# Kernel tuning notes

Hardware: AMD Instinct MI355X
Metric: run time of the kernel (lower is better)

Reference implementation:

```python
import jax, jax.numpy as jnp
import numpy as np
from jax import lax

B = 32768
IMG = 28
K = 3
OUT_HW = IMG - K + 1  # 26
FLAT = OUT_HW * OUT_HW  # 676
HID = 300
NCLS = 10


def setup_inputs() -> dict:
    key = jax.random.key(0)
    ks = jax.random.split(key, 8)
    x = jax.random.normal(ks[0], (B, IMG * IMG), dtype=jnp.float32)
    conv_w = jax.random.normal(ks[1], (K, K), dtype=jnp.float32) * 0.1
    # Linear params stored as (in, out) so forward is h @ W + b
    W1 = jax.random.normal(ks[2], (FLAT, HID), dtype=jnp.float32) * 0.04
    b1 = jnp.zeros((HID,), dtype=jnp.float32)
    W2 = jax.random.normal(ks[3], (HID, HID), dtype=jnp.float32) * 0.06
    b2 = jnp.zeros((HID,), dtype=jnp.float32)
    W3 = jax.random.normal(ks[4], (HID, NCLS), dtype=jnp.float32) * 0.06
    b3 = jnp.zeros((NCLS,), dtype=jnp.float32)
    return {"x": x, "conv_w": conv_w, "W1": W1, "b1": b1,
            "W2": W2, "b2": b2, "W3": W3, "b3": b3}


def reference(x, conv_w, W1, b1, W2, b2, W3, b3):
    b = x.shape[0]
    img = x.reshape(b, 1, IMG, IMG)  # NCHW
    # Valid cross-correlation with 3x3 kernel -> [B,1,26,26]
    y = lax.conv_general_dilated(
        img, conv_w[None, None, :, :], window_strides=(1, 1), padding="VALID",
        dimension_numbers=("NCHW", "OIHW", "NCHW"))
    h = y.reshape(b, FLAT)
    h = jax.nn.relu(h @ W1 + b1)
    h = jax.nn.relu(h @ W2 + b2)
    return h @ W3 + b3
```

## Files before the change

kernel.cpp:

```cpp
#include <hip/hip_runtime.h>


typedef __bf16 bf16_t;
typedef __bf16 bf16x4 __attribute__((ext_vector_type(4)));
typedef __bf16 bf16x8 __attribute__((ext_vector_type(8)));
typedef float  f32x4  __attribute__((ext_vector_type(4)));

#define MFMA16(a, b, c) __builtin_amdgcn_mfma_f32_16x16x32_bf16((a), (b), (c), 0, 0, 0)

#define W1F_ELEMS (25 * 20 * 64 * 8)
#define W2F_ELEMS (10 * 20 * 64 * 8)
#define W3F_ELEMS (10 * 1 * 64 * 8)
#define ASTRIDE   136

__global__ void prep_weights(const float* __restrict__ conv_w,
                             const float* __restrict__ W1,
                             const float* __restrict__ W2,
                             const float* __restrict__ W3,
                             bf16_t* __restrict__ W1f,
                             bf16_t* __restrict__ W2f,
                             bf16_t* __restrict__ W3f) {
    int idx = blockIdx.x * 256 + threadIdx.x;
    if (idx < 800 * 320) {
        int k = idx / 320;
        int n = idx - k * 320;
        float v = 0.0f;
        if (k < 784 && n < 300) {
            int py = k / 28;
            int px = k - py * 28;
#pragma unroll
            for (int ky = 0; ky < 3; ++ky) {
                int oy = py - ky;
                if (oy < 0 || oy > 25) continue;
#pragma unroll
                for (int kx = 0; kx < 3; ++kx) {
                    int ox = px - kx;
                    if (ox < 0 || ox > 25) continue;
                    v += conv_w[ky * 3 + kx] * W1[(oy * 26 + ox) * 300 + n];
                }
            }
        }
        int kc = k >> 5, quad = (k >> 3) & 3, j = k & 7;
        int nt = n >> 4, nin = n & 15;
        W1f[(((kc * 20 + nt) * 64 + quad * 16 + nin) << 3) + j] = (bf16_t)v;
    } else if (idx < 800 * 320 + 320 * 320) {
        int i2 = idx - 800 * 320;
        int k = i2 / 320;
        int n = i2 - k * 320;
        float v = (k < 300 && n < 300) ? W2[k * 300 + n] : 0.0f;
        int kc = k >> 5, quad = (k >> 3) & 3, j = k & 7;
        int nt = n >> 4, nin = n & 15;
        W2f[(((kc * 20 + nt) * 64 + quad * 16 + nin) << 3) + j] = (bf16_t)v;
    } else if (idx < 800 * 320 + 320 * 320 + 320 * 16) {
        int i3 = idx - (800 * 320 + 320 * 320);
        int k = i3 / 16;
        int n = i3 - k * 16;
        float v = (k < 300 && n < 10) ? W3[k * 10 + n] : 0.0f;
        int kc = k >> 5, quad = (k >> 3) & 3, j = k & 7;
        W3f[(((kc * 64) + quad * 16 + n) << 3) + j] = (bf16_t)v;
    }
}

__device__ __forceinline__ void stage16(const bf16x8* g, bf16x8* l) {
    __builtin_amdgcn_global_load_lds(
        (const __attribute__((address_space(1))) void*)g,
        (__attribute__((address_space(3))) void*)l, 16, 0, 0);
}

__global__ __launch_bounds__(512, 4) void fused_mlp(
    const float* __restrict__ x, const float* __restrict__ b1,
    const float* __restrict__ b2, const float* __restrict__ b3,
    const bf16x8* __restrict__ W1f, const bf16x8* __restrict__ W2f,
    const bf16x8* __restrict__ W3f, float* __restrict__ out) {
    __shared__ bf16x8 bufB1[2 * 1280];
    __shared__ bf16_t Abuf[64 * ASTRIDE];
    __shared__ bf16x8 bufB2[1280];

    bf16x8* hbuf = bufB1;

    const int tid = threadIdx.x;
    const int w   = tid >> 6;
    const int l   = tid & 63;
    const int mh  = w & 1;
    const int nq  = w >> 1;
    const int q   = l >> 4;
    const int l15 = l & 15;
    const int r0  = blockIdx.x * 64;

    const int srow = tid >> 5;
    const int sc4  = tid & 31;
    const int trow = tid >> 3;
    const int tc4  = tid & 7;

    for (int t = w; t < 20; t += 8) stage16(W1f + (t * 64 + l), bufB1 + t * 64);
    for (int t = w; t < 20; t += 8) stage16(W2f + (t * 64 + l), bufB2 + t * 64);

    float4 pf[4];
#pragma unroll
    for (int i = 0; i < 4; ++i)
        pf[i] = *(const float4*)(x + (size_t)(r0 + i * 16 + srow) * 784 + sc4 * 4);

    f32x4 acc[2][5];
#pragma unroll
    for (int m = 0; m < 2; ++m)
#pragma unroll
        for (int nt = 0; nt < 5; ++nt) acc[m][nt] = (f32x4){0.f, 0.f, 0.f, 0.f};

    int kc = 0;
    for (int band = 0; band < 7; ++band) {
        __syncthreads();

        if (band < 6) {
#pragma unroll
            for (int i = 0; i < 4; ++i) {
                bf16x4 v;
                v[0] = (bf16_t)pf[i].x; v[1] = (bf16_t)pf[i].y;
                v[2] = (bf16_t)pf[i].z; v[3] = (bf16_t)pf[i].w;
                *(bf16x4*)&Abuf[(i * 16 + srow) * ASTRIDE + sc4 * 4] = v;
            }
        } else {
            bf16x4 v;
            v[0] = (bf16_t)pf[0].x; v[1] = (bf16_t)pf[0].y;
            v[2] = (bf16_t)pf[0].z; v[3] = (bf16_t)pf[0].w;
            *(bf16x4*)&Abuf[trow * ASTRIDE + tc4 * 4] = v;
        }

        if (band + 1 < 6) {
#pragma unroll
            for (int i = 0; i < 4; ++i)
                pf[i] = *(const float4*)(x + (size_t)(r0 + i * 16 + srow) * 784 +
                                         (band + 1) * 128 + sc4 * 4);
        } else if (band + 1 == 6) {
            pf[0] = (tc4 < 4)
                ? *(const float4*)(x + (size_t)(r0 + trow) * 784 + 768 + tc4 * 4)
                : make_float4(0.f, 0.f, 0.f, 0.f);
        }

        const int nch = (band < 6) ? 4 : 1;
        for (int kcl = 0; kcl < nch; ++kcl, ++kc) {
            __syncthreads();

            if (kc + 1 < 25) {
                int s1 = (kc + 1) & 1;
                for (int t = w; t < 20; t += 8)
                    stage16(W1f + (((kc + 1) * 20 + t) * 64 + l),
                            bufB1 + s1 * 1280 + t * 64);
            }

            bf16x8 afA = *(const bf16x8*)&Abuf[(mh * 32 + l15) * ASTRIDE +
                                               kcl * 32 + q * 8];
            bf16x8 afB = *(const bf16x8*)&Abuf[(mh * 32 + 16 + l15) * ASTRIDE +
                                               kcl * 32 + q * 8];
            const bf16x8* bb = bufB1 + (kc & 1) * 1280 + (nq * 5) * 64 + l;
#pragma unroll
            for (int nt = 0; nt < 5; ++nt) {
                bf16x8 b = bb[nt * 64];
                acc[0][nt] = MFMA16(afA, b, acc[0][nt]);
                acc[1][nt] = MFMA16(afB, b, acc[1][nt]);
            }
        }
    }
    __syncthreads();

    {
        bf16_t* hb = (bf16_t*)hbuf;
#pragma unroll
        for (int nt = 0; nt < 5; ++nt) {
            int n = (nq * 5 + nt) * 16 + l15;
            float bias = (n < 300) ? b1[n] : 0.0f;
            int kc2 = n >> 5, quad = (n >> 3) & 3, j = n & 7;
#pragma unroll
            for (int mt2 = 0; mt2 < 2; ++mt2) {
                int mt = mh * 2 + mt2;
#pragma unroll
                for (int r = 0; r < 4; ++r) {
                    float v = acc[mt2][nt][r] + bias;
                    v = v > 0.f ? v : 0.f;
                    hb[(((kc2 * 4 + mt) * 64 + quad * 16 + q * 4 + r) << 3) + j] =
                        (bf16_t)v;
                }
            }
        }
    }
    __syncthreads();

#pragma unroll
    for (int m = 0; m < 2; ++m)
#pragma unroll
        for (int nt = 0; nt < 5; ++nt) acc[m][nt] = (f32x4){0.f, 0.f, 0.f, 0.f};
    for (int kc2 = 0; kc2 < 10; ++kc2) {
        bf16x8 a0 = hbuf[(kc2 * 4 + mh * 2 + 0) * 64 + l];
        bf16x8 a1 = hbuf[(kc2 * 4 + mh * 2 + 1) * 64 + l];
        const bf16x8* bb = bufB2 + (nq * 5) * 64 + l;
#pragma unroll
        for (int nt = 0; nt < 5; ++nt) {
            bf16x8 b = bb[nt * 64];
            acc[0][nt] = MFMA16(a0, b, acc[0][nt]);
            acc[1][nt] = MFMA16(a1, b, acc[1][nt]);
        }
        if (kc2 + 1 < 10) {
            __syncthreads();
            for (int t = w; t < 20; t += 8)
                stage16(W2f + (((kc2 + 1) * 20 + t) * 64 + l), bufB2 + t * 64);
            __syncthreads();
        }
    }
    __syncthreads();

    {
        bf16_t* hb = (bf16_t*)hbuf;
#pragma unroll
        for (int nt = 0; nt < 5; ++nt) {
            int n = (nq * 5 + nt) * 16 + l15;
            float bias = (n < 300) ? b2[n] : 0.0f;
            int kc2 = n >> 5, quad = (n >> 3) & 3, j = n & 7;
#pragma unroll
            for (int mt2 = 0; mt2 < 2; ++mt2) {
                int mt = mh * 2 + mt2;
#pragma unroll
                for (int r = 0; r < 4; ++r) {
                    float v = acc[mt2][nt][r] + bias;
                    v = v > 0.f ? v : 0.f;
                    hb[(((kc2 * 4 + mt) * 64 + quad * 16 + q * 4 + r) << 3) + j] =
                        (bf16_t)v;
                }
            }
        }
    }
    __syncthreads();

    if (w < 4) {
        f32x4 acc3 = (f32x4){0.f, 0.f, 0.f, 0.f};
#pragma unroll
        for (int kc3 = 0; kc3 < 10; ++kc3)
            acc3 = MFMA16(hbuf[(kc3 * 4 + w) * 64 + l], W3f[kc3 * 64 + l], acc3);
        if (l15 < 10) {
            float bias = b3[l15];
#pragma unroll
            for (int r = 0; r < 4; ++r)
                out[(size_t)(r0 + w * 16 + q * 4 + r) * 10 + l15] = acc3[r] + bias;
        }
    }
}

extern "C" void kernel_launch(void* const* d_in, const int* in_sizes, int n_in,
                              void* d_out, int out_size, void* d_ws, size_t ws_size,
                              hipStream_t stream) {
    const float* x      = (const float*)d_in[0];
    const float* conv_w = (const float*)d_in[1];
    const float* W1     = (const float*)d_in[2];
    const float* b1     = (const float*)d_in[3];
    const float* W2     = (const float*)d_in[4];
    const float* b2     = (const float*)d_in[5];
    const float* W3     = (const float*)d_in[6];
    const float* b3     = (const float*)d_in[7];
    float* out = (float*)d_out;

    char* ws = (char*)d_ws;
    bf16_t* W1f = (bf16_t*)(ws);
    bf16_t* W2f = (bf16_t*)(ws + (size_t)W1F_ELEMS * 2);
    bf16_t* W3f = (bf16_t*)(ws + (size_t)(W1F_ELEMS + W2F_ELEMS) * 2);
    if (ws_size < (size_t)(W1F_ELEMS + W2F_ELEMS + W3F_ELEMS) * 2) return;

    int prep_total = 800 * 320 + 320 * 320 + 320 * 16;
    prep_weights<<<(prep_total + 255) / 256, 256, 0, stream>>>(
        conv_w, W1, W2, W3, W1f, W2f, W3f);

    fused_mlp<<<32768 / 64, 512, 0, stream>>>(
        x, b1, b2, b3, (const bf16x8*)W1f, (const bf16x8*)W2f,
        (const bf16x8*)W3f, out);
}
```

Baseline: 187.5 us.

## Double rows per block and load weights directly into registers instead of LDS

Each block now handles 128 rows instead of 64, with each wave computing a 4x5 tile of MFMA outputs. Weight fragments for W1 and W2 are read straight from global memory (L2-resident) into registers, replacing the LDS staging, double buffering and extra barriers. LDS is merged into a single arena used for both activations and hidden layers. This raises per-wave register use, halves the block count to 256 and lowers occupancy to 2 blocks per CU. The MFMA work is no longer waiting on LDS weight staging, but each wave now issues its own global weight loads with no prefetch overlap.

```diff
diff --git a/kernel.cpp b/kernel.cpp
--- a/kernel.cpp
+++ b/kernel.cpp
@@ -61,58 +61,46 @@
     }
 }
 
-__device__ __forceinline__ void stage16(const bf16x8* g, bf16x8* l) {
-    __builtin_amdgcn_global_load_lds(
-        (const __attribute__((address_space(1))) void*)g,
-        (__attribute__((address_space(3))) void*)l, 16, 0, 0);
-}
-
-__global__ __launch_bounds__(512, 4) void fused_mlp(
+__global__ __launch_bounds__(512, 2) void fused_mlp(
     const float* __restrict__ x, const float* __restrict__ b1,
     const float* __restrict__ b2, const float* __restrict__ b3,
     const bf16x8* __restrict__ W1f, const bf16x8* __restrict__ W2f,
     const bf16x8* __restrict__ W3f, float* __restrict__ out) {
-    __shared__ bf16x8 bufB1[2 * 1280];
-    __shared__ bf16_t Abuf[64 * ASTRIDE];
-    __shared__ bf16x8 bufB2[1280];
-
-    bf16x8* hbuf = bufB1;
+    __shared__ bf16x8 arena[5120];
 
     const int tid = threadIdx.x;
     const int w   = tid >> 6;
     const int l   = tid & 63;
-    const int mh  = w & 1;
-    const int nq  = w >> 1;
     const int q   = l >> 4;
     const int l15 = l & 15;
-    const int r0  = blockIdx.x * 64;
+    const int mq  = w >> 2;
+    const int nq  = w & 3;
+    const int r0  = blockIdx.x * 128;
 
     const int srow = tid >> 5;
     const int sc4  = tid & 31;
-    const int trow = tid >> 3;
-    const int tc4  = tid & 7;
-
-    for (int t = w; t < 20; t += 8) stage16(W1f + (t * 64 + l), bufB1 + t * 64);
-    for (int t = w; t < 20; t += 8) stage16(W2f + (t * 64 + l), bufB2 + t * 64);
-
-    float4 pf[4];
-#pragma unroll
-    for (int i = 0; i < 4; ++i)
+    const int trow = tid >> 2;
+    const int tc4  = tid & 3;
+
+    bf16_t* Abuf = (bf16_t*)arena;
+
+    float4 pf[8];
+#pragma unroll
+    for (int i = 0; i < 8; ++i)
         pf[i] = *(const float4*)(x + (size_t)(r0 + i * 16 + srow) * 784 + sc4 * 4);
 
-    f32x4 acc[2][5];
-#pragma unroll
-    for (int m = 0; m < 2; ++m)
-#pragma unroll
-        for (int nt = 0; nt < 5; ++nt) acc[m][nt] = (f32x4){0.f, 0.f, 0.f, 0.f};
-
-    int kc = 0;
+    f32x4 acc1[4][5];
+#pragma unroll
+    for (int mt = 0; mt < 4; ++mt)
+#pragma unroll
+        for (int nt = 0; nt < 5; ++nt) acc1[mt][nt] = (f32x4){0.f, 0.f, 0.f, 0.f};
+
     for (int band = 0; band < 7; ++band) {
         __syncthreads();
 
         if (band < 6) {
 #pragma unroll
-            for (int i = 0; i < 4; ++i) {
+            for (int i = 0; i < 8; ++i) {
                 bf16x4 v;
                 v[0] = (bf16_t)pf[i].x; v[1] = (bf16_t)pf[i].y;
                 v[2] = (bf16_t)pf[i].z; v[3] = (bf16_t)pf[i].w;
@@ -123,60 +111,54 @@
             v[0] = (bf16_t)pf[0].x; v[1] = (bf16_t)pf[0].y;
             v[2] = (bf16_t)pf[0].z; v[3] = (bf16_t)pf[0].w;
             *(bf16x4*)&Abuf[trow * ASTRIDE + tc4 * 4] = v;
-        }
+            bf16x4 z = (bf16x4){(bf16_t)0.f, (bf16_t)0.f, (bf16_t)0.f, (bf16_t)0.f};
+            *(bf16x4*)&Abuf[trow * ASTRIDE + 16 + tc4 * 4] = z;
+        }
+        __syncthreads();
 
         if (band + 1 < 6) {
 #pragma unroll
-            for (int i = 0; i < 4; ++i)
+            for (int i = 0; i < 8; ++i)
                 pf[i] = *(const float4*)(x + (size_t)(r0 + i * 16 + srow) * 784 +
                                          (band + 1) * 128 + sc4 * 4);
         } else if (band + 1 == 6) {
-            pf[0] = (tc4 < 4)
-                ? *(const float4*)(x + (size_t)(r0 + trow) * 784 + 768 + tc4 * 4)
-                : make_float4(0.f, 0.f, 0.f, 0.f);
+            pf[0] = *(const float4*)(x + (size_t)(r0 + trow) * 784 + 768 + tc4 * 4);
         }
 
         const int nch = (band < 6) ? 4 : 1;
-        for (int kcl = 0; kcl < nch; ++kcl, ++kc) {
-            __syncthreads();
-
-            if (kc + 1 < 25) {
-                int s1 = (kc + 1) & 1;
-                for (int t = w; t < 20; t += 8)
-                    stage16(W1f + (((kc + 1) * 20 + t) * 64 + l),
-                            bufB1 + s1 * 1280 + t * 64);
-            }
-
-            bf16x8 afA = *(const bf16x8*)&Abuf[(mh * 32 + l15) * ASTRIDE +
-                                               kcl * 32 + q * 8];
-            bf16x8 afB = *(const bf16x8*)&Abuf[(mh * 32 + 16 + l15) * ASTRIDE +
-                                               kcl * 32 + q * 8];
-            const bf16x8* bb = bufB1 + (kc & 1) * 1280 + (nq * 5) * 64 + l;
-#pragma unroll
-            for (int nt = 0; nt < 5; ++nt) {
-                bf16x8 b = bb[nt * 64];
-                acc[0][nt] = MFMA16(afA, b, acc[0][nt]);
-                acc[1][nt] = MFMA16(afB, b, acc[1][nt]);
+        for (int kcl = 0; kcl < nch; ++kcl) {
+            const int kc = band * 4 + kcl;
+            bf16x8 bfr[5];
+            const bf16x8* wb = W1f + ((size_t)kc * 20 + nq * 5) * 64 + l;
+#pragma unroll
+            for (int nt = 0; nt < 5; ++nt) bfr[nt] = wb[nt * 64];
+#pragma unroll
+            for (int mt = 0; mt < 4; ++mt) {
+                bf16x8 a = *(const bf16x8*)&Abuf[(mq * 64 + mt * 16 + l15) * ASTRIDE +
+                                                 kcl * 32 + q * 8];
+#pragma unroll
+                for (int nt = 0; nt < 5; ++nt)
+                    acc1[mt][nt] = MFMA16(a, bfr[nt], acc1[mt][nt]);
             }
         }
     }
     __syncthreads();
 
     {
-        bf16_t* hb = (bf16_t*)hbuf;
+        bf16_t* hb = (bf16_t*)arena;
 #pragma unroll
         for (int nt = 0; nt < 5; ++nt) {
-            int n = (nq * 5 + nt) * 16 + l15;
+            int n = nq * 80 + nt * 16 + l15;
             float bias = (n < 300) ? b1[n] : 0.0f;
             int kc2 = n >> 5, quad = (n >> 3) & 3, j = n & 7;
 #pragma unroll
-            for (int mt2 = 0; mt2 < 2; ++mt2) {
-                int mt = mh * 2 + mt2;
+            for (int mt = 0; mt < 4; ++mt) {
+                int mtg = mq * 4 + mt;
 #pragma unroll
                 for (int r = 0; r < 4; ++r) {
-                    float v = acc[mt2][nt][r] + bias;
+                    float v = acc1[mt][nt][r] + bias;
                     v = v > 0.f ? v : 0.f;
-                    hb[(((kc2 * 4 + mt) * 64 + quad * 16 + q * 4 + r) << 3) + j] =
+                    hb[(((kc2 * 8 + mtg) * 64 + quad * 16 + q * 4 + r) << 3) + j] =
                         (bf16_t)v;
                 }
             }
@@ -184,44 +166,41 @@
     }
     __syncthreads();
 
-#pragma unroll
-    for (int m = 0; m < 2; ++m)
-#pragma unroll
-        for (int nt = 0; nt < 5; ++nt) acc[m][nt] = (f32x4){0.f, 0.f, 0.f, 0.f};
-    for (int kc2 = 0; kc2 < 10; ++kc2) {
-        bf16x8 a0 = hbuf[(kc2 * 4 + mh * 2 + 0) * 64 + l];
-        bf16x8 a1 = hbuf[(kc2 * 4 + mh * 2 + 1) * 64 + l];
-        const bf16x8* bb = bufB2 + (nq * 5) * 64 + l;
+    f32x4 acc2[4][5];
+#pragma unroll
+    for (int mt = 0; mt < 4; ++mt)
+#pragma unroll
+        for (int nt = 0; nt < 5; ++nt) acc2[mt][nt] = (f32x4){0.f, 0.f, 0.f, 0.f};
+    for (int kc = 0; kc < 10; ++kc) {
+        bf16x8 b2f[5];
+        const bf16x8* wb = W2f + ((size_t)kc * 20 + nq * 5) * 64 + l;
+#pragma unroll
+        for (int nt = 0; nt < 5; ++nt) b2f[nt] = wb[nt * 64];
+#pragma unroll
+        for (int mt = 0; mt < 4; ++mt) {
+            bf16x8 a = arena[(kc * 8 + mq * 4 + mt) * 64 + l];
+#pragma unroll
+            for (int nt = 0; nt < 5; ++nt)
+                acc2[mt][nt] = MFMA16(a, b2f[nt], acc2[mt][nt]);
+        }
+    }
+    __syncthreads();
+
+    {
+        bf16_t* hb = (bf16_t*)arena;
 #pragma unroll
         for (int nt = 0; nt < 5; ++nt) {
-            bf16x8 b = bb[nt * 64];
-            acc[0][nt] = MFMA16(a0, b, acc[0][nt]);
-            acc[1][nt] = MFMA16(a1, b, acc[1][nt]);
-        }
-        if (kc2 + 1 < 10) {
-            __syncthreads();
-            for (int t = w; t < 20; t += 8)
-                stage16(W2f + (((kc2 + 1) * 20 + t) * 64 + l), bufB2 + t * 64);
-            __syncthreads();
-        }
-    }
-    __syncthreads();
-
-    {
-        bf16_t* hb = (bf16_t*)hbuf;
-#pragma unroll
-        for (int nt = 0; nt < 5; ++nt) {
-            int n = (nq * 5 + nt) * 16 + l15;
+            int n = nq * 80 + nt * 16 + l15;
             float bias = (n < 300) ? b2[n] : 0.0f;
             int kc2 = n >> 5, quad = (n >> 3) & 3, j = n & 7;
 #pragma unroll
-            for (int mt2 = 0; mt2 < 2; ++mt2) {
-                int mt = mh * 2 + mt2;
+            for (int mt = 0; mt < 4; ++mt) {
+                int mtg = mq * 4 + mt;
 #pragma unroll
                 for (int r = 0; r < 4; ++r) {
-                    float v = acc[mt2][nt][r] + bias;
+                    float v = acc2[mt][nt][r] + bias;
                     v = v > 0.f ? v : 0.f;
-                    hb[(((kc2 * 4 + mt) * 64 + quad * 16 + q * 4 + r) << 3) + j] =
+                    hb[(((kc2 * 8 + mtg) * 64 + quad * 16 + q * 4 + r) << 3) + j] =
                         (bf16_t)v;
                 }
             }
@@ -229,17 +208,15 @@
     }
     __syncthreads();
 
-    if (w < 4) {
-        f32x4 acc3 = (f32x4){0.f, 0.f, 0.f, 0.f};
-#pragma unroll
-        for (int kc3 = 0; kc3 < 10; ++kc3)
-            acc3 = MFMA16(hbuf[(kc3 * 4 + w) * 64 + l], W3f[kc3 * 64 + l], acc3);
-        if (l15 < 10) {
-            float bias = b3[l15];
-#pragma unroll
-            for (int r = 0; r < 4; ++r)
-                out[(size_t)(r0 + w * 16 + q * 4 + r) * 10 + l15] = acc3[r] + bias;
-        }
+    f32x4 acc3 = (f32x4){0.f, 0.f, 0.f, 0.f};
+#pragma unroll
+    for (int kc = 0; kc < 10; ++kc)
+        acc3 = MFMA16(arena[(kc * 8 + w) * 64 + l], W3f[kc * 64 + l], acc3);
+    if (l15 < 10) {
+        float bias = b3[l15];
+#pragma unroll
+        for (int r = 0; r < 4; ++r)
+            out[(size_t)(r0 + w * 16 + q * 4 + r) * 10 + l15] = acc3[r] + bias;
     }
 }
 
@@ -266,7 +243,7 @@
     prep_weights<<<(prep_total + 255) / 256, 256, 0, stream>>>(
         conv_w, W1, W2, W3, W1f, W2f, W3f);
 
-    fused_mlp<<<32768 / 64, 512, 0, stream>>>(
+    fused_mlp<<<32768 / 128, 512, 0, stream>>>(
         x, b1, b2, b3, (const bf16x8*)W1f, (const bf16x8*)W2f,
         (const bf16x8*)W3f, out);
 }
```

Result: no change. 189.7 us (+1.1%).

## Pre-convert input to bf16 MFMA fragment layout and load operands directly from global

Applied to the files above, without the earlier changes.

Adds a separate kernel that converts x to bf16 and rearranges it into MFMA fragment order in workspace. The main kernel then reads A and B fragments straight from global memory into registers with double-buffered prefetch, so it no longer stages through LDS and drops most __syncthreads. Launch bounds occupancy is lowered to 2. The cost is an extra pass that writes and rereads x in bf16, plus every block reading the weights from L2 instead of sharing them through LDS.

```diff
diff --git a/kernel.cpp b/kernel.cpp
--- a/kernel.cpp
+++ b/kernel.cpp
@@ -11,7 +11,8 @@
 #define W1F_ELEMS (25 * 20 * 64 * 8)
 #define W2F_ELEMS (10 * 20 * 64 * 8)
 #define W3F_ELEMS (10 * 1 * 64 * 8)
-#define ASTRIDE   136
+#define XF_OFF    768000
+#define XF_BYTES  ((size_t)2048 * 25 * 64 * 16)
 
 __global__ void prep_weights(const float* __restrict__ conv_w,
                              const float* __restrict__ W1,
@@ -61,22 +62,43 @@
     }
 }
 
-__device__ __forceinline__ void stage16(const bf16x8* g, bf16x8* l) {
-    __builtin_amdgcn_global_load_lds(
-        (const __attribute__((address_space(1))) void*)g,
-        (__attribute__((address_space(3))) void*)l, 16, 0, 0);
-}
-
-__global__ __launch_bounds__(512, 4) void fused_mlp(
-    const float* __restrict__ x, const float* __restrict__ b1,
+#define XMAIN (32768 * 196)
+#define XZERO (2048 * 32 * 2)
+
+__global__ void xconvert(const float* __restrict__ x, bf16_t* __restrict__ xf) {
+    int idx = blockIdx.x * 256 + threadIdx.x;
+    if (idx < XMAIN) {
+        float4 v = ((const float4*)x)[idx];
+        int row = idx / 196;
+        int c4  = idx - row * 196;
+        int t = row >> 4, l15 = row & 15;
+        int kc = c4 >> 3, q = (c4 >> 1) & 3, half = c4 & 1;
+        bf16x4 o;
+        o[0] = (bf16_t)v.x; o[1] = (bf16_t)v.y;
+        o[2] = (bf16_t)v.z; o[3] = (bf16_t)v.w;
+        size_t slot = ((size_t)t * 25 + kc) * 64 + q * 16 + l15;
+        *(bf16x4*)(xf + slot * 8 + half * 4) = o;
+    } else {
+        int z = idx - XMAIN;
+        if (z < XZERO) {
+            int half = z & 1;
+            int z2 = z >> 1;
+            int t = z2 >> 5;
+            int r5 = z2 & 31;
+            int qq = r5 >> 4, l15 = r5 & 15;
+            size_t slot = ((size_t)t * 25 + 24) * 64 + (2 + qq) * 16 + l15;
+            bf16x4 o = (bf16x4){(bf16_t)0.f, (bf16_t)0.f, (bf16_t)0.f, (bf16_t)0.f};
+            *(bf16x4*)(xf + slot * 8 + half * 4) = o;
+        }
+    }
+}
+
+__global__ __launch_bounds__(512, 2) void fused_mlp(
+    const bf16x8* __restrict__ xf, const float* __restrict__ b1,
     const float* __restrict__ b2, const float* __restrict__ b3,
     const bf16x8* __restrict__ W1f, const bf16x8* __restrict__ W2f,
     const bf16x8* __restrict__ W3f, float* __restrict__ out) {
-    __shared__ bf16x8 bufB1[2 * 1280];
-    __shared__ bf16_t Abuf[64 * ASTRIDE];
-    __shared__ bf16x8 bufB2[1280];
-
-    bf16x8* hbuf = bufB1;
+    __shared__ bf16x8 hbuf[10 * 4 * 64];
 
     const int tid = threadIdx.x;
     const int w   = tid >> 6;
@@ -87,18 +109,9 @@
     const int l15 = l & 15;
     const int r0  = blockIdx.x * 64;
 
-    const int srow = tid >> 5;
-    const int sc4  = tid & 31;
-    const int trow = tid >> 3;
-    const int tc4  = tid & 7;
-
-    for (int t = w; t < 20; t += 8) stage16(W1f + (t * 64 + l), bufB1 + t * 64);
-    for (int t = w; t < 20; t += 8) stage16(W2f + (t * 64 + l), bufB2 + t * 64);
-
-    float4 pf[4];
-#pragma unroll
-    for (int i = 0; i < 4; ++i)
-        pf[i] = *(const float4*)(x + (size_t)(r0 + i * 16 + srow) * 784 + sc4 * 4);
+    const bf16x8* xa0 = xf + ((size_t)(blockIdx.x * 4 + mh * 2 + 0) * 25) * 64 + l;
+    const bf16x8* xa1 = xf + ((size_t)(blockIdx.x * 4 + mh * 2 + 1) * 25) * 64 + l;
+    const bf16x8* wb1 = W1f + (nq * 5) * 64 + l;
 
     f32x4 acc[2][5];
 #pragma unroll
@@ -106,61 +119,27 @@
 #pragma unroll
         for (int nt = 0; nt < 5; ++nt) acc[m][nt] = (f32x4){0.f, 0.f, 0.f, 0.f};
 
-    int kc = 0;
-    for (int band = 0; band < 7; ++band) {
-        __syncthreads();
-
-        if (band < 6) {
-#pragma unroll
-            for (int i = 0; i < 4; ++i) {
-                bf16x4 v;
-                v[0] = (bf16_t)pf[i].x; v[1] = (bf16_t)pf[i].y;
-                v[2] = (bf16_t)pf[i].z; v[3] = (bf16_t)pf[i].w;
-                *(bf16x4*)&Abuf[(i * 16 + srow) * ASTRIDE + sc4 * 4] = v;
-            }
-        } else {
-            bf16x4 v;
-            v[0] = (bf16_t)pf[0].x; v[1] = (bf16_t)pf[0].y;
-            v[2] = (bf16_t)pf[0].z; v[3] = (bf16_t)pf[0].w;
-            *(bf16x4*)&Abuf[trow * ASTRIDE + tc4 * 4] = v;
-        }
-
-        if (band + 1 < 6) {
-#pragma unroll
-            for (int i = 0; i < 4; ++i)
-                pf[i] = *(const float4*)(x + (size_t)(r0 + i * 16 + srow) * 784 +
-                                         (band + 1) * 128 + sc4 * 4);
-        } else if (band + 1 == 6) {
-            pf[0] = (tc4 < 4)
-                ? *(const float4*)(x + (size_t)(r0 + trow) * 784 + 768 + tc4 * 4)
-                : make_float4(0.f, 0.f, 0.f, 0.f);
-        }
-
-        const int nch = (band < 6) ? 4 : 1;
-        for (int kcl = 0; kcl < nch; ++kcl, ++kc) {
-            __syncthreads();
-
-            if (kc + 1 < 25) {
-                int s1 = (kc + 1) & 1;
-                for (int t = w; t < 20; t += 8)
-                    stage16(W1f + (((kc + 1) * 20 + t) * 64 + l),
-                            bufB1 + s1 * 1280 + t * 64);
-            }
-
-            bf16x8 afA = *(const bf16x8*)&Abuf[(mh * 32 + l15) * ASTRIDE +
-                                               kcl * 32 + q * 8];
-            bf16x8 afB = *(const bf16x8*)&Abuf[(mh * 32 + 16 + l15) * ASTRIDE +
-                                               kcl * 32 + q * 8];
-            const bf16x8* bb = bufB1 + (kc & 1) * 1280 + (nq * 5) * 64 + l;
-#pragma unroll
-            for (int nt = 0; nt < 5; ++nt) {
-                bf16x8 b = bb[nt * 64];
-                acc[0][nt] = MFMA16(afA, b, acc[0][nt]);
-                acc[1][nt] = MFMA16(afB, b, acc[1][nt]);
-            }
-        }
-    }
-    __syncthreads();
+    bf16x8 a0[2], a1[2], bfr[2][5];
+    a0[0] = xa0[0];
+    a1[0] = xa1[0];
+#pragma unroll
+    for (int nt = 0; nt < 5; ++nt) bfr[0][nt] = wb1[nt * 64];
+
+    for (int kc = 0; kc < 25; ++kc) {
+        const int cur = kc & 1, nxt = cur ^ 1;
+        if (kc + 1 < 25) {
+            a0[nxt] = xa0[(kc + 1) * 64];
+            a1[nxt] = xa1[(kc + 1) * 64];
+            const bf16x8* wb = wb1 + (size_t)(kc + 1) * 20 * 64;
+#pragma unroll
+            for (int nt = 0; nt < 5; ++nt) bfr[nxt][nt] = wb[nt * 64];
+        }
+#pragma unroll
+        for (int nt = 0; nt < 5; ++nt) {
+            acc[0][nt] = MFMA16(a0[cur], bfr[cur][nt], acc[0][nt]);
+            acc[1][nt] = MFMA16(a1[cur], bfr[cur][nt], acc[1][nt]);
+        }
+    }
 
     {
         bf16_t* hb = (bf16_t*)hbuf;
@@ -188,21 +167,24 @@
     for (int m = 0; m < 2; ++m)
 #pragma unroll
         for (int nt = 0; nt < 5; ++nt) acc[m][nt] = (f32x4){0.f, 0.f, 0.f, 0.f};
-    for (int kc2 = 0; kc2 < 10; ++kc2) {
-        bf16x8 a0 = hbuf[(kc2 * 4 + mh * 2 + 0) * 64 + l];
-        bf16x8 a1 = hbuf[(kc2 * 4 + mh * 2 + 1) * 64 + l];
-        const bf16x8* bb = bufB2 + (nq * 5) * 64 + l;
-#pragma unroll
-        for (int nt = 0; nt < 5; ++nt) {
-            bf16x8 b = bb[nt * 64];
-            acc[0][nt] = MFMA16(a0, b, acc[0][nt]);
-            acc[1][nt] = MFMA16(a1, b, acc[1][nt]);
-        }
-        if (kc2 + 1 < 10) {
-            __syncthreads();
-            for (int t = w; t < 20; t += 8)
-                stage16(W2f + (((kc2 + 1) * 20 + t) * 64 + l), bufB2 + t * 64);
-            __syncthreads();
+    const bf16x8* wb2 = W2f + (nq * 5) * 64 + l;
+    bf16x8 b2f[2][5];
+#pragma unroll
+    for (int nt = 0; nt < 5; ++nt) b2f[0][nt] = wb2[nt * 64];
+
+    for (int kc = 0; kc < 10; ++kc) {
+        const int cur = kc & 1, nxt = cur ^ 1;
+        if (kc + 1 < 10) {
+            const bf16x8* wb = wb2 + (size_t)(kc + 1) * 20 * 64;
+#pragma unroll
+            for (int nt = 0; nt < 5; ++nt) b2f[nxt][nt] = wb[nt * 64];
+        }
+        bf16x8 ha0 = hbuf[(kc * 4 + mh * 2 + 0) * 64 + l];
+        bf16x8 ha1 = hbuf[(kc * 4 + mh * 2 + 1) * 64 + l];
+#pragma unroll
+        for (int nt = 0; nt < 5; ++nt) {
+            acc[0][nt] = MFMA16(ha0, b2f[cur][nt], acc[0][nt]);
+            acc[1][nt] = MFMA16(ha1, b2f[cur][nt], acc[1][nt]);
         }
     }
     __syncthreads();
@@ -232,8 +214,8 @@
     if (w < 4) {
         f32x4 acc3 = (f32x4){0.f, 0.f, 0.f, 0.f};
 #pragma unroll
-        for (int kc3 = 0; kc3 < 10; ++kc3)
-            acc3 = MFMA16(hbuf[(kc3 * 4 + w) * 64 + l], W3f[kc3 * 64 + l], acc3);
+        for (int kc = 0; kc < 10; ++kc)
+            acc3 = MFMA16(hbuf[(kc * 4 + w) * 64 + l], W3f[kc * 64 + l], acc3);
         if (l15 < 10) {
             float bias = b3[l15];
 #pragma unroll
@@ -260,13 +242,16 @@
     bf16_t* W1f = (bf16_t*)(ws);
     bf16_t* W2f = (bf16_t*)(ws + (size_t)W1F_ELEMS * 2);
     bf16_t* W3f = (bf16_t*)(ws + (size_t)(W1F_ELEMS + W2F_ELEMS) * 2);
-    if (ws_size < (size_t)(W1F_ELEMS + W2F_ELEMS + W3F_ELEMS) * 2) return;
+    bf16_t* xf  = (bf16_t*)(ws + XF_OFF);
+    if (ws_size < XF_OFF + XF_BYTES) return;
 
     int prep_total = 800 * 320 + 320 * 320 + 320 * 16;
     prep_weights<<<(prep_total + 255) / 256, 256, 0, stream>>>(
         conv_w, W1, W2, W3, W1f, W2f, W3f);
 
+    xconvert<<<(XMAIN + XZERO) / 256, 256, 0, stream>>>(x, xf);
+
     fused_mlp<<<32768 / 64, 512, 0, stream>>>(
-        x, b1, b2, b3, (const bf16x8*)W1f, (const bf16x8*)W2f,
-        (const bf16x8*)W3f, out);
-}
+        (const bf16x8*)xf, b1, b2, b3, (const bf16x8*)W1f,
+        (const bf16x8*)W2f, (const bf16x8*)W3f, out);
+}
```

New measurement: 231.5 us. 1.23x slower.
